# Performance work log

Hardware: AMD Instinct MI355X
Metric: run time of the kernel (lower is better)

Reference implementation:

```python
import jax, jax.numpy as jnp
import numpy as np

CASCADING_LOSS = 0.85


def _bilinear_sample(img, px, py):
    """grid_sample(align_corners=True, padding_mode='zeros') in pixel coords.
    img: [B,C,H,W]; px,py: [B,H,W] absolute pixel coordinates."""
    B, C, H, W = img.shape
    x0 = jnp.floor(px)
    y0 = jnp.floor(py)
    x1 = x0 + 1.0
    y1 = y0 + 1.0
    wx1 = px - x0
    wx0 = 1.0 - wx1
    wy1 = py - y0
    wy0 = 1.0 - wy1

    def gather(yi, xi):
        valid = (xi >= 0) & (xi <= W - 1) & (yi >= 0) & (yi <= H - 1)
        xc = jnp.clip(xi, 0, W - 1).astype(jnp.int32)
        yc = jnp.clip(yi, 0, H - 1).astype(jnp.int32)
        # per-batch advanced indexing: [B,C,H,W]
        vals = jax.vmap(lambda im, yy, xx: im[:, yy, xx])(img, yc, xc)
        return vals * valid[:, None, :, :].astype(img.dtype)

    out = (gather(y0, x0) * (wy0 * wx0)[:, None, :, :]
           + gather(y0, x1) * (wy0 * wx1)[:, None, :, :]
           + gather(y1, x0) * (wy1 * wx0)[:, None, :, :]
           + gather(y1, x1) * (wy1 * wx1)[:, None, :, :])
    return out


def _add_flow(img, flw):
    # img: [B,C,H,W]; flw: [B,2,H,W] with channel 0 -> y offset, channel 1 -> x offset
    B, C, H, W = img.shape
    base_x = jnp.arange(W, dtype=img.dtype)[None, None, :]   # [1,1,W]
    base_y = jnp.arange(H, dtype=img.dtype)[None, :, None]   # [1,H,1]
    px = base_x + flw[:, 1, :, :]
    py = base_y + flw[:, 0, :, :]
    return _bilinear_sample(img, px, py)


def _compute_psnr(target, estim):
    mse = jnp.mean((target - estim) ** 2)
    return 10.0 * jnp.log(1.0 / mse) / jnp.log(jnp.asarray(10.0, target.dtype))


def setup_inputs() -> dict:
    key = jax.random.key(0)
    k1, k2, k3 = jax.random.split(key, 3)
    ITERS, B, H, W, C = 12, 4, 384, 512, 3
    flow_tup = jax.random.normal(k1, (ITERS, B, 2, H, W), dtype=jnp.float32)
    frame1 = jax.random.uniform(k2, (B, C, H, W), dtype=jnp.float32)
    frame2 = jax.random.uniform(k3, (B, C, H, W), dtype=jnp.float32)
    return {"flow_tup": flow_tup, "frame1": frame1, "frame2": frame2}


def reference(flow_tup, frame1, frame2):
    n_iters = flow_tup.shape[0]
    # vectorize warp over GRU iterations
    estims = jax.vmap(lambda f: _add_flow(frame1, f))(flow_tup)  # [I,B,C,H,W]
    psnrs = jax.vmap(lambda e: _compute_psnr(frame2, e))(estims)  # [I]
    weights = CASCADING_LOSS ** (n_iters - jnp.arange(n_iters, dtype=flow_tup.dtype))
    loss = -jnp.sum(psnrs * weights)
    return loss
```

## Files before the change

### kernel.cpp

```cpp
#include <hip/hip_runtime.h>
#include <math.h>

typedef _Float16 h2 __attribute__((ext_vector_type(2)));

static __device__ __forceinline__ h2 pkrtz(float a, float b) {
    return __builtin_bit_cast(h2, __builtin_amdgcn_cvt_pkrtz(a, b));
}

#define ITERS 12
#define BATCH 4
#define CH 3
#define H 384
#define W 512

constexpr int HW  = H * W;
constexpr int CHW = CH * HW;
constexpr int TILE_X = 32, TILE_Y = 16;
constexpr int TX_N = W / TILE_X;
constexpr int TY_N = H / TILE_Y;
constexpr int NBLK = BATCH * TX_N * TY_N;
constexpr int HALO = 8;
constexpr int WIN_W = TILE_X + 2 * HALO;
constexpr int WIN_H = TILE_Y + 2 * HALO;
constexpr int WIN_CELLS = WIN_W * WIN_H;
constexpr int FSTRIDE = BATCH * 2 * HW;

__global__ __launch_bounds__(256, 8) void warp_mse_kernel(
    const float* __restrict__ flow,
    const float* __restrict__ f1,
    const float* __restrict__ f2,
    float* __restrict__ partials)
{
    __shared__ uint2 win[WIN_CELLS];

    int tid = threadIdx.x;
    int bx  = blockIdx.x;
    int b   = bx / (TX_N * TY_N);
    int t   = bx - b * (TX_N * TY_N);
    int ty  = t / TX_N;
    int tx  = t - ty * TX_N;
    int x_t = tx * TILE_X, y_t = ty * TILE_Y;

    const float* f1b = f1 + b * CHW;
    const float* f2b = f2 + b * CHW;

#pragma unroll
    for (int k = 0; k < 3; ++k) {
        int q   = tid + 256 * k;
        int row = q / (WIN_W / 2);
        int cp  = q - row * (WIN_W / 2);
        int gx0 = x_t - HALO + 2 * cp;
        int gxc = min(max(gx0, 0), W - 2);
        int gy  = min(max(y_t - HALO + row, 0), H - 1);
        const float* src = f1b + gy * W + gxc;
        float2 c0 = *(const float2*)(src);
        float2 c1 = *(const float2*)(src + HW);
        float2 c2 = *(const float2*)(src + 2 * HW);
        unsigned a0 = __builtin_bit_cast(unsigned, pkrtz(c0.x, c1.x));
        unsigned b0 = __builtin_bit_cast(unsigned, pkrtz(c2.x, 0.0f));
        unsigned a1 = __builtin_bit_cast(unsigned, pkrtz(c0.y, c1.y));
        unsigned b1 = __builtin_bit_cast(unsigned, pkrtz(c2.y, 0.0f));
        int wb = row * WIN_W + 2 * cp;
        win[wb]     = make_uint2(a0, b0);
        win[wb + 1] = make_uint2(a1, b1);
    }
    __syncthreads();

    int x = x_t + 2 * (tid & 15);
    int y = y_t + (tid >> 4);
    int p = y * W + x;
    float yf = (float)y;

    float2 tc0 = *(const float2*)(f2b + p);
    float2 tc1 = *(const float2*)(f2b + HW + p);
    float2 tc2 = *(const float2*)(f2b + 2 * HW + p);
    h2 t01[2], t2p[2];
    t01[0] = pkrtz(tc0.x, tc1.x);
    t2p[0] = pkrtz(tc2.x, 0.0f);
    t01[1] = pkrtz(tc0.y, tc1.y);
    t2p[1] = pkrtz(tc2.y, 0.0f);

    alignas(16) float acc[ITERS];
#pragma unroll
    for (int k = 0; k < ITERS; ++k) acc[k] = 0.0f;

    const float* fp = flow + b * 2 * HW + p;
    float2 fy0 = *(const float2*)(fp);
    float2 fx0 = *(const float2*)(fp + HW);
    float2 fy1 = *(const float2*)(fp + FSTRIDE);
    float2 fx1 = *(const float2*)(fp + FSTRIDE + HW);

#pragma unroll
    for (int it = 0; it < ITERS; ++it) {
        const float* fp2 = fp + 2 * FSTRIDE;
        float2 fy2 = make_float2(0.0f, 0.0f), fx2 = make_float2(0.0f, 0.0f);
        if (it + 2 < ITERS) { fy2 = *(const float2*)(fp2); fx2 = *(const float2*)(fp2 + HW); }

        float a_it = 0.0f;
#pragma unroll
        for (int j = 0; j < 2; ++j) {
            float fy = j ? fy0.y : fy0.x;
            float fx = j ? fx0.y : fx0.x;
            float pxf = (float)(x + j) + fx;
            float pyf = yf + fy;
            float x0f = floorf(pxf), y0f = floorf(pyf);
            float wx1 = pxf - x0f, wy1 = pyf - y0f;
            float wx0 = 1.0f - wx1, wy0 = 1.0f - wy1;
            int x0 = (int)x0f, y0 = (int)y0f;
            int x1 = x0 + 1,  y1 = y0 + 1;

            bool vx0 = (x0 >= 0) & (x0 <= W - 1);
            bool vx1 = (x1 >= 0) & (x1 <= W - 1);
            bool vy0 = (y0 >= 0) & (y0 <= H - 1);
            bool vy1 = (y1 >= 0) & (y1 <= H - 1);

            float w00 = wy0 * wx0 * (float)(vy0 && vx0);
            float w01 = wy0 * wx1 * (float)(vy0 && vx1);
            float w10 = wy1 * wx0 * (float)(vy1 && vx0);
            float w11 = wy1 * wx1 * (float)(vy1 && vx1);

            int lx0 = x0 - (x_t - HALO);
            int ly0 = y0 - (y_t - HALO);
            int a   = ly0 * WIN_W + lx0;
            a = min(max(a, 0), WIN_CELLS - WIN_W - 2);

            uint2 c00 = win[a];
            uint2 c10 = win[a + WIN_W];
            uint2 c01 = win[a + 1];
            uint2 c11 = win[a + WIN_W + 1];

            h2 w00h = pkrtz(w00, w00);
            h2 w01h = pkrtz(w01, w01);
            h2 w10h = pkrtz(w10, w10);
            h2 w11h = pkrtz(w11, w11);

            h2 v01 = __builtin_bit_cast(h2, c00.x) * w00h
                   + __builtin_bit_cast(h2, c01.x) * w01h
                   + __builtin_bit_cast(h2, c10.x) * w10h
                   + __builtin_bit_cast(h2, c11.x) * w11h;
            h2 v2  = __builtin_bit_cast(h2, c00.y) * w00h
                   + __builtin_bit_cast(h2, c01.y) * w01h
                   + __builtin_bit_cast(h2, c10.y) * w10h
                   + __builtin_bit_cast(h2, c11.y) * w11h;

            h2 d01 = t01[j] - v01;
            h2 d2  = t2p[j] - v2;
            a_it += (float)d01.x * (float)d01.x + (float)d01.y * (float)d01.y
                  + (float)d2.x * (float)d2.x;
        }
        acc[it] = a_it;
        fy0 = fy1; fx0 = fx1; fy1 = fy2; fx1 = fx2; fp += FSTRIDE;
    }

    __syncthreads();
    float* scr = (float*)win;
    float4* sc4 = (float4*)scr;
    const float4* av = (const float4*)acc;
    sc4[tid * 3 + 0] = av[0];
    sc4[tid * 3 + 1] = av[1];
    sc4[tid * 3 + 2] = av[2];
    __syncthreads();

    int lane = tid & 63;
    int wv   = tid >> 6;
#pragma unroll
    for (int r = 0; r < 3; ++r) {
        int k = wv + 4 * r;
        float s = scr[lane * 12 + k]
                + scr[(lane + 64) * 12 + k]
                + scr[(lane + 128) * 12 + k]
                + scr[(lane + 192) * 12 + k];
#pragma unroll
        for (int off = 32; off > 0; off >>= 1)
            s += __shfl_down(s, off, 64);
        if (lane == 0) partials[k * NBLK + bx] = s;
    }
}

__global__ __launch_bounds__(768) void finalize_kernel(
    const float* __restrict__ partials,
    float* __restrict__ out)
{
    __shared__ float psnr_w[ITERS];
    int wave = threadIdx.x >> 6;
    int lane = threadIdx.x & 63;

    float s = 0.0f;
    const float* pp = partials + wave * NBLK;
    for (int j = lane; j < NBLK; j += 64)
        s += pp[j];
#pragma unroll
    for (int off = 32; off > 0; off >>= 1)
        s += __shfl_down(s, off, 64);

    if (lane == 0) {
        float mse  = s * (1.0f / (float)(BATCH * CH * HW));
        float psnr = -10.0f * 0.30102999566398f * log2f(mse);
        float w = 1.0f;
        for (int k = 0; k < ITERS - wave; ++k) w *= 0.85f;
        psnr_w[wave] = psnr * w;
    }
    __syncthreads();
    if (threadIdx.x == 0) {
        float loss = 0.0f;
#pragma unroll
        for (int i = 0; i < ITERS; ++i) loss += psnr_w[i];
        out[0] = -loss;
    }
}

extern "C" void kernel_launch(void* const* d_in, const int* in_sizes, int n_in,
                              void* d_out, int out_size, void* d_ws, size_t ws_size,
                              hipStream_t stream) {
    const float* flow = (const float*)d_in[0];
    const float* f1   = (const float*)d_in[1];
    const float* f2   = (const float*)d_in[2];
    float* out        = (float*)d_out;
    float* partials   = (float*)d_ws;

    warp_mse_kernel<<<NBLK, 256, 0, stream>>>(flow, f1, f2, partials);
    finalize_kernel<<<1, 768, 0, stream>>>(partials, out);
}
```

Before: 134.2 us.

## Fuse finalize into warp kernel via atomics, specialize interior tiles, deepen prefetch

Removes the separate finalize kernel. Each block now atomically adds its per-iteration sums into double accumulators, and the last block, found with a global counter, computes the loss. Interior tiles skip the zero-padding validity checks through a template specialization, and flow prefetch is deepened from two iterations ahead to three. A memset is added to clear the accumulators each launch. The double atomics add contention across many blocks.

Measured after the change: 272.9 us. 2.03x slower.

```diff
diff --git a/kernel.cpp b/kernel.cpp
--- a/kernel.cpp
+++ b/kernel.cpp
@@ -25,11 +25,70 @@
 constexpr int WIN_CELLS = WIN_W * WIN_H;
 constexpr int FSTRIDE = BATCH * 2 * HW;
 
+template <bool INTERIOR>
+static __device__ __forceinline__ float tap_px(
+    const uint2* __restrict__ win, int xg, float yf, float fx, float fy,
+    int x_t, int y_t, h2 t01, h2 t2p)
+{
+    float pxf = (float)xg + fx;
+    float pyf = yf + fy;
+    float x0f = floorf(pxf), y0f = floorf(pyf);
+    float wx1 = pxf - x0f, wy1 = pyf - y0f;
+    float wx0 = 1.0f - wx1, wy0 = 1.0f - wy1;
+    int x0 = (int)x0f, y0 = (int)y0f;
+
+    float w00 = wy0 * wx0;
+    float w01 = wy0 * wx1;
+    float w10 = wy1 * wx0;
+    float w11 = wy1 * wx1;
+
+    if (!INTERIOR) {
+        int x1 = x0 + 1, y1 = y0 + 1;
+        bool vx0 = (x0 >= 0) & (x0 <= W - 1);
+        bool vx1 = (x1 >= 0) & (x1 <= W - 1);
+        bool vy0 = (y0 >= 0) & (y0 <= H - 1);
+        bool vy1 = (y1 >= 0) & (y1 <= H - 1);
+        w00 *= (float)(vy0 && vx0);
+        w01 *= (float)(vy0 && vx1);
+        w10 *= (float)(vy1 && vx0);
+        w11 *= (float)(vy1 && vx1);
+    }
+
+    int a = (y0 - (y_t - HALO)) * WIN_W + (x0 - (x_t - HALO));
+    a = min(max(a, 0), WIN_CELLS - WIN_W - 2);
+
+    uint2 c00 = win[a];
+    uint2 c10 = win[a + WIN_W];
+    uint2 c01 = win[a + 1];
+    uint2 c11 = win[a + WIN_W + 1];
+
+    h2 w00h = pkrtz(w00, w00);
+    h2 w01h = pkrtz(w01, w01);
+    h2 w10h = pkrtz(w10, w10);
+    h2 w11h = pkrtz(w11, w11);
+
+    h2 v01 = __builtin_bit_cast(h2, c00.x) * w00h
+           + __builtin_bit_cast(h2, c01.x) * w01h
+           + __builtin_bit_cast(h2, c10.x) * w10h
+           + __builtin_bit_cast(h2, c11.x) * w11h;
+    h2 v2  = __builtin_bit_cast(h2, c00.y) * w00h
+           + __builtin_bit_cast(h2, c01.y) * w01h
+           + __builtin_bit_cast(h2, c10.y) * w10h
+           + __builtin_bit_cast(h2, c11.y) * w11h;
+
+    h2 d01 = t01 - v01;
+    h2 d2  = t2p - v2;
+    return (float)d01.x * (float)d01.x + (float)d01.y * (float)d01.y
+         + (float)d2.x * (float)d2.x;
+}
+
 __global__ __launch_bounds__(256, 8) void warp_mse_kernel(
     const float* __restrict__ flow,
     const float* __restrict__ f1,
     const float* __restrict__ f2,
-    float* __restrict__ partials)
+    double* __restrict__ sums,
+    unsigned* __restrict__ counter,
+    float* __restrict__ out)
 {
     __shared__ uint2 win[WIN_CELLS];
 
@@ -40,6 +99,7 @@
     int ty  = t / TX_N;
     int tx  = t - ty * TX_N;
     int x_t = tx * TILE_X, y_t = ty * TILE_Y;
+    bool interior = (tx > 0) & (tx < TX_N - 1) & (ty > 0) & (ty < TY_N - 1);
 
     const float* f1b = f1 + b * CHW;
     const float* f2b = f2 + b * CHW;
@@ -74,82 +134,40 @@
     float2 tc0 = *(const float2*)(f2b + p);
     float2 tc1 = *(const float2*)(f2b + HW + p);
     float2 tc2 = *(const float2*)(f2b + 2 * HW + p);
-    h2 t01[2], t2p[2];
-    t01[0] = pkrtz(tc0.x, tc1.x);
-    t2p[0] = pkrtz(tc2.x, 0.0f);
-    t01[1] = pkrtz(tc0.y, tc1.y);
-    t2p[1] = pkrtz(tc2.y, 0.0f);
+    h2 t01a = pkrtz(tc0.x, tc1.x), t2pa = pkrtz(tc2.x, 0.0f);
+    h2 t01b = pkrtz(tc0.y, tc1.y), t2pb = pkrtz(tc2.y, 0.0f);
 
     alignas(16) float acc[ITERS];
 #pragma unroll
     for (int k = 0; k < ITERS; ++k) acc[k] = 0.0f;
 
     const float* fp = flow + b * 2 * HW + p;
-    float2 fy0 = *(const float2*)(fp);
-    float2 fx0 = *(const float2*)(fp + HW);
-    float2 fy1 = *(const float2*)(fp + FSTRIDE);
-    float2 fx1 = *(const float2*)(fp + FSTRIDE + HW);
+    float2 fyq[3], fxq[3];
+#pragma unroll
+    for (int k = 0; k < 3; ++k) {
+        fyq[k] = *(const float2*)(fp + k * FSTRIDE);
+        fxq[k] = *(const float2*)(fp + k * FSTRIDE + HW);
+    }
 
 #pragma unroll
     for (int it = 0; it < ITERS; ++it) {
-        const float* fp2 = fp + 2 * FSTRIDE;
-        float2 fy2 = make_float2(0.0f, 0.0f), fx2 = make_float2(0.0f, 0.0f);
-        if (it + 2 < ITERS) { fy2 = *(const float2*)(fp2); fx2 = *(const float2*)(fp2 + HW); }
-
-        float a_it = 0.0f;
-#pragma unroll
-        for (int j = 0; j < 2; ++j) {
-            float fy = j ? fy0.y : fy0.x;
-            float fx = j ? fx0.y : fx0.x;
-            float pxf = (float)(x + j) + fx;
-            float pyf = yf + fy;
-            float x0f = floorf(pxf), y0f = floorf(pyf);
-            float wx1 = pxf - x0f, wy1 = pyf - y0f;
-            float wx0 = 1.0f - wx1, wy0 = 1.0f - wy1;
-            int x0 = (int)x0f, y0 = (int)y0f;
-            int x1 = x0 + 1,  y1 = y0 + 1;
-
-            bool vx0 = (x0 >= 0) & (x0 <= W - 1);
-            bool vx1 = (x1 >= 0) & (x1 <= W - 1);
-            bool vy0 = (y0 >= 0) & (y0 <= H - 1);
-            bool vy1 = (y1 >= 0) & (y1 <= H - 1);
-
-            float w00 = wy0 * wx0 * (float)(vy0 && vx0);
-            float w01 = wy0 * wx1 * (float)(vy0 && vx1);
-            float w10 = wy1 * wx0 * (float)(vy1 && vx0);
-            float w11 = wy1 * wx1 * (float)(vy1 && vx1);
-
-            int lx0 = x0 - (x_t - HALO);
-            int ly0 = y0 - (y_t - HALO);
-            int a   = ly0 * WIN_W + lx0;
-            a = min(max(a, 0), WIN_CELLS - WIN_W - 2);
-
-            uint2 c00 = win[a];
-            uint2 c10 = win[a + WIN_W];
-            uint2 c01 = win[a + 1];
-            uint2 c11 = win[a + WIN_W + 1];
-
-            h2 w00h = pkrtz(w00, w00);
-            h2 w01h = pkrtz(w01, w01);
-            h2 w10h = pkrtz(w10, w10);
-            h2 w11h = pkrtz(w11, w11);
-
-            h2 v01 = __builtin_bit_cast(h2, c00.x) * w00h
-                   + __builtin_bit_cast(h2, c01.x) * w01h
-                   + __builtin_bit_cast(h2, c10.x) * w10h
-                   + __builtin_bit_cast(h2, c11.x) * w11h;
-            h2 v2  = __builtin_bit_cast(h2, c00.y) * w00h
-                   + __builtin_bit_cast(h2, c01.y) * w01h
-                   + __builtin_bit_cast(h2, c10.y) * w10h
-                   + __builtin_bit_cast(h2, c11.y) * w11h;
-
-            h2 d01 = t01[j] - v01;
-            h2 d2  = t2p[j] - v2;
-            a_it += (float)d01.x * (float)d01.x + (float)d01.y * (float)d01.y
-                  + (float)d2.x * (float)d2.x;
+        const float* fp3 = fp + 3 * FSTRIDE;
+        float2 fyn = make_float2(0.0f, 0.0f), fxn = make_float2(0.0f, 0.0f);
+        if (it + 3 < ITERS) { fyn = *(const float2*)(fp3); fxn = *(const float2*)(fp3 + HW); }
+
+        float a_it;
+        if (interior) {
+            a_it = tap_px<true >(win, x,     yf, fxq[0].x, fyq[0].x, x_t, y_t, t01a, t2pa)
+                 + tap_px<true >(win, x + 1, yf, fxq[0].y, fyq[0].y, x_t, y_t, t01b, t2pb);
+        } else {
+            a_it = tap_px<false>(win, x,     yf, fxq[0].x, fyq[0].x, x_t, y_t, t01a, t2pa)
+                 + tap_px<false>(win, x + 1, yf, fxq[0].y, fyq[0].y, x_t, y_t, t01b, t2pb);
         }
         acc[it] = a_it;
-        fy0 = fy1; fx0 = fx1; fy1 = fy2; fx1 = fx2; fp += FSTRIDE;
+        fyq[0] = fyq[1]; fxq[0] = fxq[1];
+        fyq[1] = fyq[2]; fxq[1] = fxq[2];
+        fyq[2] = fyn;    fxq[2] = fxn;
+        fp += FSTRIDE;
     }
 
     __syncthreads();
@@ -173,39 +191,27 @@
 #pragma unroll
         for (int off = 32; off > 0; off >>= 1)
             s += __shfl_down(s, off, 64);
-        if (lane == 0) partials[k * NBLK + bx] = s;
-    }
-}
-
-__global__ __launch_bounds__(768) void finalize_kernel(
-    const float* __restrict__ partials,
-    float* __restrict__ out)
-{
-    __shared__ float psnr_w[ITERS];
-    int wave = threadIdx.x >> 6;
-    int lane = threadIdx.x & 63;
-
-    float s = 0.0f;
-    const float* pp = partials + wave * NBLK;
-    for (int j = lane; j < NBLK; j += 64)
-        s += pp[j];
-#pragma unroll
-    for (int off = 32; off > 0; off >>= 1)
-        s += __shfl_down(s, off, 64);
-
-    if (lane == 0) {
-        float mse  = s * (1.0f / (float)(BATCH * CH * HW));
-        float psnr = -10.0f * 0.30102999566398f * log2f(mse);
-        float w = 1.0f;
-        for (int k = 0; k < ITERS - wave; ++k) w *= 0.85f;
-        psnr_w[wave] = psnr * w;
-    }
-    __syncthreads();
-    if (threadIdx.x == 0) {
-        float loss = 0.0f;
-#pragma unroll
-        for (int i = 0; i < ITERS; ++i) loss += psnr_w[i];
-        out[0] = -loss;
+        if (lane == 0) atomicAdd(&sums[k], (double)s);
+    }
+
+    __syncthreads();
+    if (tid == 0) {
+        __threadfence();
+        unsigned old = atomicAdd(counter, 1u);
+        if (old == NBLK - 1) {
+            double loss = 0.0;
+            const float inv_n = 1.0f / (float)(BATCH * CH * HW);
+            float w = 1.0f;
+#pragma unroll
+            for (int i = ITERS - 1; i >= 0; --i) {
+                double tot = atomicAdd(&sums[i], 0.0);
+                float mse  = (float)tot * inv_n;
+                float psnr = -10.0f * 0.30102999566398f * log2f(mse);
+                w = (i == ITERS - 1) ? 0.85f : w * 0.85f;
+                loss += (double)(psnr * w);
+            }
+            out[0] = -(float)loss;
+        }
     }
 }
 
@@ -216,8 +222,9 @@
     const float* f1   = (const float*)d_in[1];
     const float* f2   = (const float*)d_in[2];
     float* out        = (float*)d_out;
-    float* partials   = (float*)d_ws;
-
-    warp_mse_kernel<<<NBLK, 256, 0, stream>>>(flow, f1, f2, partials);
-    finalize_kernel<<<1, 768, 0, stream>>>(partials, out);
-}
+    double* sums      = (double*)d_ws;
+    unsigned* counter = (unsigned*)((char*)d_ws + 96);
+
+    hipMemsetAsync(d_ws, 0, 128, stream);
+    warp_mse_kernel<<<NBLK, 256, 0, stream>>>(flow, f1, f2, sums, counter, out);
+}
```
